# Performance work log

Hardware: AMD Instinct MI355X
Metric: run time of the kernel (lower is better)

## Reference

```python
import jax, jax.numpy as jnp
import numpy as np

N = 2708
IN_CH = 1433
OUT_CH = 128
NEG_SLOPE = 0.2


def setup_inputs() -> dict:
    key = jax.random.key(0)
    ks = jax.random.split(key, 7)
    X = jax.random.normal(ks[0], (N, IN_CH), dtype=jnp.float32)
    A = jax.random.randint(ks[1], (N, N), 0, 2, dtype=jnp.int32)
    U = jax.random.normal(ks[2], (N, N), dtype=jnp.float32)
    W = jax.random.normal(ks[3], (OUT_CH, IN_CH), dtype=jnp.float32) * (1.0 / np.sqrt(IN_CH))
    a1 = jax.random.normal(ks[4], (1, OUT_CH), dtype=jnp.float32) * (1.0 / np.sqrt(OUT_CH))
    a2 = jax.random.normal(ks[5], (1, OUT_CH), dtype=jnp.float32) * (1.0 / np.sqrt(OUT_CH))
    lmbd = jax.random.normal(ks[6], (N, 1), dtype=jnp.float32)
    return {"X": X, "A": A, "U": U, "W": W, "a1": a1, "a2": a2, "lmbd": lmbd}


def reference(X, A, U, W, a1, a2, lmbd):
    # K = W(X): [N, out]
    K = X @ W.T
    k1 = K @ a1.T                      # [N, 1]
    k2 = K @ a2.T                      # [N, 1]
    E = k1 + k2.T                      # [N, N] broadcast sum
    # spectral filter: igft(lmbd * gft(E)) = U @ (lmbd * (U^T @ E))
    E = jnp.abs(U @ (lmbd * (U.T @ E)))
    E = jnp.where(E >= 0, E, NEG_SLOPE * E)  # leaky_relu
    E_masked = jnp.where(A == 0, -jnp.inf, E)
    alpha = jax.nn.softmax(E_masked, axis=-1)  # row-wise masked softmax
    # dropout p=0.0 (eval) -> identity
    H = alpha @ K                      # [N, out]
    return H
```

## Files before the change

kernel.cpp:

```cpp
#include <hip/hip_runtime.h>
#include <math.h>

#define NN 2708
#define IC 1433
#define OC 128
#define NV (NN / 4)
#define NNOC ((size_t)NN * OC)
#define NW 85

__global__ __launch_bounds__(256) void prep2(const float* __restrict__ W, float* __restrict__ Wt,
                                             const float* __restrict__ a1, const float* __restrict__ a2,
                                             double* __restrict__ w1, double* __restrict__ w2,
                                             double* __restrict__ zd, int nzd) {
  __shared__ float tile[32][33];
  const int b = blockIdx.x, t = threadIdx.x;
  if (b < 180) {
    const int k0 = (b % 45) * 32, o0 = (b / 45) * 32;
#pragma unroll
    for (int it = 0; it < 4; it++) {
      int ro = (t >> 5) + it * 8;
      int k  = k0 + (t & 31);
      tile[ro][t & 31] = (k < IC) ? W[(size_t)(o0 + ro) * IC + k] : 0.f;
    }
    __syncthreads();
#pragma unroll
    for (int it = 0; it < 4; it++) {
      int rk = (t >> 5) + it * 8;
      int k  = k0 + rk;
      if (k < IC) Wt[(size_t)k * OC + o0 + (t & 31)] = tile[t & 31][rk];
    }
  } else if (b < 186) {
    float* a1s = &tile[0][0];
    float* a2s = a1s + 128;
    if (t < 128) { a1s[t] = a1[t]; a2s[t] = a2[t]; }
    __syncthreads();
    int c = (b - 180) * 256 + t;
    if (c < IC) {
      const float* Wc = W + c;
      double s1 = 0.0, s2 = 0.0;
#pragma unroll 4
      for (int o = 0; o < OC; o++) {
        double w = (double)Wc[(size_t)o * IC];
        s1 = fma(w, (double)a1s[o], s1);
        s2 = fma(w, (double)a2s[o], s2);
      }
      w1[c] = s1; w2[c] = s2;
    }
  } else {
    int gid = (b - 186) * 256 + t;
    if (gid < nzd) zd[gid] = 0.0;
  }
}

__global__ __launch_bounds__(256) void xw_gemm(const float* __restrict__ X,
                                               const double* __restrict__ w1, const double* __restrict__ w2,
                                               double* __restrict__ k1, double* __restrict__ k2,
                                               const float* __restrict__ Wt, float* __restrict__ Kp,
                                               const int* __restrict__ A, unsigned* __restrict__ bm,
                                               int chunk, int nsplit) {
  __shared__ __align__(16) char smem[21504];
  const int b = blockIdx.x, t = threadIdx.x;
  const int ngm = 85 * nsplit;
  if (b < ngm) {
    float (*Xs)[36]  = (float (*)[36])smem;
    float (*Ws)[132] = (float (*)[132])(smem + 32 * 36 * 4);
    const int bx = b % 85, by = b / 85;
    const int rb = bx * 32;
    const int ks = by * chunk;
    const int ke = min(IC, ks + chunk);
    float* __restrict__ Ko = Kp + (size_t)by * NNOC;
    const int row0 = (t >> 5) * 4;
    const int col4 = (t & 31) * 4;
    float acc[4][4];
#pragma unroll
    for (int r = 0; r < 4; r++)
#pragma unroll
      for (int c = 0; c < 4; c++) acc[r][c] = 0.f;

    for (int kb = ks; kb < ke; kb += 32) {
#pragma unroll
      for (int it = 0; it < 4; it++) {
        int idx = t + it * 256;
        int r = idx >> 5, c = idx & 31;
        int gr = rb + r, gc = kb + c;
        Xs[r][c] = (gr < NN && gc < ke) ? X[(size_t)gr * IC + gc] : 0.f;
      }
#pragma unroll
      for (int it = 0; it < 4; it++) {
        int idx4 = t + it * 256;
        int k = idx4 >> 5, cg = (idx4 & 31) * 4;
        int gk = kb + k;
        float4 v = make_float4(0.f, 0.f, 0.f, 0.f);
        if (gk < ke) v = *reinterpret_cast<const float4*>(&Wt[(size_t)gk * OC + cg]);
        *reinterpret_cast<float4*>(&Ws[k][cg]) = v;
      }
      __syncthreads();
#pragma unroll
      for (int g = 0; g < 8; g++) {
        float xr[4][4];
#pragma unroll
        for (int r = 0; r < 4; r++)
          *reinterpret_cast<float4*>(xr[r]) = *reinterpret_cast<const float4*>(&Xs[row0 + r][g * 4]);
#pragma unroll
        for (int j = 0; j < 4; j++) {
          const float4 w4 = *reinterpret_cast<const float4*>(&Ws[g * 4 + j][col4]);
#pragma unroll
          for (int r = 0; r < 4; r++) {
            acc[r][0] = fmaf(xr[r][j], w4.x, acc[r][0]);
            acc[r][1] = fmaf(xr[r][j], w4.y, acc[r][1]);
            acc[r][2] = fmaf(xr[r][j], w4.z, acc[r][2]);
            acc[r][3] = fmaf(xr[r][j], w4.w, acc[r][3]);
          }
        }
      }
      __syncthreads();
    }
#pragma unroll
    for (int r = 0; r < 4; r++) {
      int gr = rb + row0 + r;
      if (gr < NN) {
        float4 v = make_float4(acc[r][0], acc[r][1], acc[r][2], acc[r][3]);
        *reinterpret_cast<float4*>(&Ko[(size_t)gr * OC + col4]) = v;
      }
    }
  } else if (b < ngm + 900) {
    const int bb = b - ngm;
    int gid = bb * 256 + t;
    const int total = NN * NW;
    if (gid >= total) return;
    int i = gid / NW, w = gid - i * NW;
    const int* Ar = A + (size_t)i * NN + w * 32;
    unsigned word = 0;
    if (w < NW - 1) {
      const int4* a4 = (const int4*)Ar;
#pragma unroll
      for (int u = 0; u < 8; u++) {
        int4 a = a4[u];
        word |= (a.x != 0 ? 1u : 0u) << (4 * u);
        word |= (a.y != 0 ? 1u : 0u) << (4 * u + 1);
        word |= (a.z != 0 ? 1u : 0u) << (4 * u + 2);
        word |= (a.w != 0 ? 1u : 0u) << (4 * u + 3);
      }
    } else {
      const int nbits = NN - w * 32;
      for (int bb2 = 0; bb2 < nbits; bb2++) word |= (Ar[bb2] != 0 ? 1u : 0u) << bb2;
    }
    bm[(size_t)i * NW + w] = word;
  } else {
    const int bb = b - ngm - 900;
    const int wave = t >> 6, lane = t & 63;
    const int i = bb * 4 + wave;
    if (i >= NN) return;
    const float* Xi = X + (size_t)i * IC;
    double s1 = 0.0, s2 = 0.0;
    for (int c = lane; c < IC; c += 64) {
      double x = (double)Xi[c];
      s1 = fma(x, w1[c], s1);
      s2 = fma(x, w2[c], s2);
    }
    for (int o = 32; o; o >>= 1) { s1 += __shfl_down(s1, o, 64); s2 += __shfl_down(s2, o, 64); }
    if (lane == 0) { k1[i] = s1; k2[i] = s2; }
  }
}

__global__ __launch_bounds__(256) void mid(const float4* __restrict__ U4, const double* __restrict__ k1,
                                           double* __restrict__ u1, double* __restrict__ s,
                                           const float4* __restrict__ Kp4, float4* __restrict__ Kf4,
                                           int nsplit) {
  const int b = blockIdx.x, t = threadIdx.x;
  if (b < 255) {
    const int slab = b / 3, chunk = b - slab * 3;
    const int c4 = chunk * 256 + t;
    if (c4 >= NV) return;
    const int r0 = slab * 32;
    const int r1 = min(NN, r0 + 32);
    double au0 = 0, au1_ = 0, au2 = 0, au3 = 0, as0 = 0, as1 = 0, as2 = 0, as3 = 0;
#pragma unroll 4
    for (int r = r0; r < r1; r++) {
      float4 u = U4[(size_t)r * NV + c4];
      double kr = k1[r];
      au0 = fma((double)u.x, kr, au0); au1_ = fma((double)u.y, kr, au1_);
      au2 = fma((double)u.z, kr, au2); au3 = fma((double)u.w, kr, au3);
      as0 += (double)u.x; as1 += (double)u.y; as2 += (double)u.z; as3 += (double)u.w;
    }
    int c = c4 * 4;
    atomicAdd(&u1[c + 0], au0); atomicAdd(&u1[c + 1], au1_);
    atomicAdd(&u1[c + 2], au2); atomicAdd(&u1[c + 3], au3);
    atomicAdd(&s[c + 0], as0);  atomicAdd(&s[c + 1], as1);
    atomicAdd(&s[c + 2], as2);  atomicAdd(&s[c + 3], as3);
  } else {
    size_t i = (size_t)(b - 255) * 256 + t;
    const size_t n4 = NNOC / 4;
    if (i >= n4) return;
    float4 sv;
    if (nsplit == 4) {
      float4 v[4];
#pragma unroll
      for (int pp = 0; pp < 4; pp++) v[pp] = Kp4[(size_t)pp * n4 + i];
      sv = v[0];
#pragma unroll
      for (int pp = 1; pp < 4; pp++) {
        sv.x += v[pp].x; sv.y += v[pp].y; sv.z += v[pp].z; sv.w += v[pp].w;
      }
    } else {
      sv = Kp4[i];
      for (int pp = 1; pp < nsplit; pp++) {
        float4 v = Kp4[(size_t)pp * n4 + i];
        sv.x += v.x; sv.y += v.y; sv.z += v.z; sv.w += v.w;
      }
    }
    Kf4[i] = sv;
  }
}

__global__ __launch_bounds__(256) void softuvH(const unsigned* __restrict__ bm,
                                               const float4* __restrict__ U4, const float4* __restrict__ L4,
                                               const double2* __restrict__ u1d, const double2* __restrict__ sd,
                                               const double* __restrict__ k2,
                                               const float* __restrict__ K, float* __restrict__ H) {
  __shared__ float vf[NN];
  __shared__ short js[NN];
  __shared__ float hpart[4][128];
  __shared__ unsigned bmr[NW];
  __shared__ double redd[4], redp[4], redq[4];
  __shared__ float redf[4];
  __shared__ int cntS;

  const int i = blockIdx.x;
  const int t = threadIdx.x;
  const int wv = t >> 6, lane = t & 63;
  const unsigned long long ltmask = (1ull << lane) - 1ull;

  if (t < NW) bmr[t] = bm[(size_t)i * NW + t];
  if (t == 0) cntS = 0;

  const float4* Ur = U4 + (size_t)i * NV;
  double ap = 0.0, aq = 0.0;
  for (int c4 = t; c4 < NV; c4 += 256) {
    float4 u = Ur[c4];
    float4 lm = L4[c4];
    double2 ua = u1d[c4 * 2], ub = u1d[c4 * 2 + 1];
    double2 sa = sd[c4 * 2],  sb = sd[c4 * 2 + 1];
    ap = fma((double)u.x, (double)lm.x * ua.x, ap);
    ap = fma((double)u.y, (double)lm.y * ua.y, ap);
    ap = fma((double)u.z, (double)lm.z * ub.x, ap);
    ap = fma((double)u.w, (double)lm.w * ub.y, ap);
    aq = fma((double)u.x, (double)lm.x * sa.x, aq);
    aq = fma((double)u.y, (double)lm.y * sa.y, aq);
    aq = fma((double)u.z, (double)lm.z * sb.x, aq);
    aq = fma((double)u.w, (double)lm.w * sb.y, aq);
  }
  for (int o = 32; o; o >>= 1) { ap += __shfl_down(ap, o, 64); aq += __shfl_down(aq, o, 64); }
  if (lane == 0) { redp[wv] = ap; redq[wv] = aq; }
  __syncthreads();
  const double pi = (redp[0] + redp[1]) + (redp[2] + redp[3]);
  const double qi = (redq[0] + redq[1]) + (redq[2] + redq[3]);

  double m = -1e300;
  for (int j = t; j < NN; j += 256) {
    if ((bmr[j >> 5] >> (j & 31)) & 1u) {
      double v = fma(qi, k2[j], pi);
      m = fmax(m, fabs(v));
    }
  }
  for (int o = 32; o; o >>= 1) m = fmax(m, __shfl_xor(m, o, 64));
  if (lane == 0) redd[wv] = m;
  __syncthreads();
  m = fmax(fmax(redd[0], redd[1]), fmax(redd[2], redd[3]));

  const double thr = m - 21.0;
  float sw = 0.f;
  for (int j = t; j < NN; j += 256) {
    bool keep = false;
    double av = 0.0;
    if ((bmr[j >> 5] >> (j & 31)) & 1u) {
      av = fabs(fma(qi, k2[j], pi));
      keep = (av > thr);
    }
    unsigned long long mask = __ballot(keep);
    if (mask) {
      int src = __ffsll(mask) - 1;
      int basew = 0;
      if (lane == src) basew = atomicAdd(&cntS, __popcll(mask));
      basew = __shfl(basew, src, 64);
      if (keep) {
        int pos = basew + __popcll(mask & ltmask);
        float w = __expf((float)(av - m));
        js[pos] = (short)j;
        vf[pos] = w;
        sw += w;
      }
    }
  }
  for (int o = 32; o; o >>= 1) sw += __shfl_xor(sw, o, 64);
  if (lane == 0) redf[wv] = sw;
  __syncthreads();
  const float sumw = (redf[0] + redf[1]) + (redf[2] + redf[3]);
  const int nlist = cntS;

  const int ch = t & 63, g = t >> 6;
  float a0 = 0.f, a1 = 0.f;
  int c = g;
  for (; c + 28 < nlist; c += 32) {
    float wr[8]; int jr[8];
#pragma unroll
    for (int u = 0; u < 8; u++) { wr[u] = vf[c + 4 * u]; jr[u] = js[c + 4 * u]; }
    float kl[8], kh[8];
#pragma unroll
    for (int u = 0; u < 8; u++) {
      const float* Kr = K + (size_t)jr[u] * OC;
      kl[u] = Kr[ch]; kh[u] = Kr[64 + ch];
    }
#pragma unroll
    for (int u = 0; u < 8; u++) { a0 = fmaf(wr[u], kl[u], a0); a1 = fmaf(wr[u], kh[u], a1); }
  }
  for (; c < nlist; c += 4) {
    float w = vf[c];
    const float* Kr = K + (size_t)js[c] * OC;
    a0 = fmaf(w, Kr[ch], a0);
    a1 = fmaf(w, Kr[64 + ch], a1);
  }
  hpart[g][ch] = a0;
  hpart[g][64 + ch] = a1;
  __syncthreads();
  if (t < 128) {
    float hv = (hpart[0][t] + hpart[1][t]) + (hpart[2][t] + hpart[3][t]);
    H[(size_t)i * OC + t] = hv / sumw;
  }
}

extern "C" void kernel_launch(void* const* d_in, const int* in_sizes, int n_in,
                              void* d_out, int out_size, void* d_ws, size_t ws_size,
                              hipStream_t stream) {
  const float* X    = (const float*)d_in[0];
  const int*   A    = (const int*)d_in[1];
  const float* U    = (const float*)d_in[2];
  const float* W    = (const float*)d_in[3];
  const float* a1   = (const float*)d_in[4];
  const float* a2   = (const float*)d_in[5];
  const float* lmbd = (const float*)d_in[6];
  float* H = (float*)d_out;

  const size_t wt_bytes  = (size_t)IC * OC * 4;
  const size_t bm_bytes  = (size_t)NN * NW * 4;
  const size_t dbl_bytes = (size_t)(6 * NN + 2 * IC) * 8;

  const int splits[3] = {4, 2, 1};
  int nsplit = 1;
  for (int ci = 0; ci < 3; ci++) {
    int ns = splits[ci];
    size_t need = (size_t)(ns > 1 ? ns + 1 : 1) * NNOC * 4 + wt_bytes + dbl_bytes +
                  bm_bytes + 1024;
    if (need <= ws_size) { nsplit = ns; break; }
  }

  char* base = (char*)d_ws;
  float* Kp = (float*)base;
  float* Kf = (nsplit > 1) ? (float*)(base + (size_t)nsplit * NNOC * 4) : Kp;
  size_t off = (size_t)(nsplit > 1 ? nsplit + 1 : 1) * NNOC * 4;
  float* Wt = (float*)(base + off);            off += wt_bytes;
  double* dbl = (double*)(base + off);         off += dbl_bytes;
  double* k1  = dbl;
  double* k2  = k1 + NN;
  double* u1  = k2 + NN;
  double* sC  = u1 + NN;
  double* w1  = sC + NN + 2 * NN;
  double* w2  = w1 + IC;
  unsigned* bm = (unsigned*)(base + off);      off += bm_bytes;

  const int chunk = (IC + nsplit - 1) / nsplit;
  const int nmerge = (int)((NNOC / 4 + 255) / 256);

  prep2<<<208, 256, 0, stream>>>(W, Wt, a1, a2, w1, w2, u1, 2 * NN);
  xw_gemm<<<85 * nsplit + 900 + 677, 256, 0, stream>>>(X, w1, w2, k1, k2, Wt, Kp, A, bm,
                                                       chunk, nsplit);
  mid<<<255 + (nsplit > 1 ? nmerge : 0), 256, 0, stream>>>((const float4*)U, k1, u1, sC,
                                                           (const float4*)Kp, (float4*)Kf, nsplit);
  softuvH<<<NN, 256, 0, stream>>>(bm, (const float4*)U, (const float4*)lmbd,
                                  (const double2*)u1, (const double2*)sC, k2, Kf, H);
}
```

Baseline: 211.1 us.

## Split-K GEMM into 16 chunks with atomic accumulation, drop merge pass

Raises the split-K factor of the X·W GEMM from at most 4 to 16 (chunk of 90 along K). Partial results are now accumulated with float atomics into a buffer that prep2 zeroes, so the separate partial-sum merge in mid and its workspace go away. The k1/k2 row reduction also stages w1/w2 in shared memory. This gives more GEMM blocks for occupancy, but adds heavy float atomic traffic and makes the summation order nondeterministic.

```diff
diff --git a/kernel.cpp b/kernel.cpp
--- a/kernel.cpp
+++ b/kernel.cpp
@@ -7,11 +7,13 @@
 #define NV (NN / 4)
 #define NNOC ((size_t)NN * OC)
 #define NW 85
+#define NSPLIT 16
+#define CHUNK 90
 
 __global__ __launch_bounds__(256) void prep2(const float* __restrict__ W, float* __restrict__ Wt,
                                              const float* __restrict__ a1, const float* __restrict__ a2,
                                              double* __restrict__ w1, double* __restrict__ w2,
-                                             double* __restrict__ zd, int nzd) {
+                                             double* __restrict__ zd, float4* __restrict__ Kf4) {
   __shared__ float tile[32][33];
   const int b = blockIdx.x, t = threadIdx.x;
   if (b < 180) {
@@ -46,29 +48,30 @@
       }
       w1[c] = s1; w2[c] = s2;
     }
+  } else if (b < 208) {
+    int gid = (b - 186) * 256 + t;
+    if (gid < 2 * NN) zd[gid] = 0.0;
   } else {
-    int gid = (b - 186) * 256 + t;
-    if (gid < nzd) zd[gid] = 0.0;
+    size_t gid = (size_t)(b - 208) * 256 + t;
+    if (gid < NNOC / 4) Kf4[gid] = make_float4(0.f, 0.f, 0.f, 0.f);
   }
 }
 
 __global__ __launch_bounds__(256) void xw_gemm(const float* __restrict__ X,
                                                const double* __restrict__ w1, const double* __restrict__ w2,
                                                double* __restrict__ k1, double* __restrict__ k2,
-                                               const float* __restrict__ Wt, float* __restrict__ Kp,
-                                               const int* __restrict__ A, unsigned* __restrict__ bm,
-                                               int chunk, int nsplit) {
-  __shared__ __align__(16) char smem[21504];
+                                               const float* __restrict__ Wt, float* __restrict__ Kf,
+                                               const int* __restrict__ A, unsigned* __restrict__ bm) {
+  __shared__ __align__(16) char smem[23040];
   const int b = blockIdx.x, t = threadIdx.x;
-  const int ngm = 85 * nsplit;
+  const int ngm = 85 * NSPLIT;
   if (b < ngm) {
     float (*Xs)[36]  = (float (*)[36])smem;
     float (*Ws)[132] = (float (*)[132])(smem + 32 * 36 * 4);
     const int bx = b % 85, by = b / 85;
     const int rb = bx * 32;
-    const int ks = by * chunk;
-    const int ke = min(IC, ks + chunk);
-    float* __restrict__ Ko = Kp + (size_t)by * NNOC;
+    const int ks = by * CHUNK;
+    const int ke = min(IC, ks + CHUNK);
     const int row0 = (t >> 5) * 4;
     const int col4 = (t & 31) * 4;
     float acc[4][4];
@@ -119,8 +122,9 @@
     for (int r = 0; r < 4; r++) {
       int gr = rb + row0 + r;
       if (gr < NN) {
-        float4 v = make_float4(acc[r][0], acc[r][1], acc[r][2], acc[r][3]);
-        *reinterpret_cast<float4*>(&Ko[(size_t)gr * OC + col4]) = v;
+        float* Ko = &Kf[(size_t)gr * OC + col4];
+#pragma unroll
+        for (int cc = 0; cc < 4; cc++) atomicAdd(&Ko[cc], acc[r][cc]);
       }
     }
   } else if (b < ngm + 900) {
@@ -148,6 +152,10 @@
     bm[(size_t)i * NW + w] = word;
   } else {
     const int bb = b - ngm - 900;
+    double* w1s = (double*)smem;
+    double* w2s = w1s + IC;
+    for (int c = t; c < IC; c += 256) { w1s[c] = w1[c]; w2s[c] = w2[c]; }
+    __syncthreads();
     const int wave = t >> 6, lane = t & 63;
     const int i = bb * 4 + wave;
     if (i >= NN) return;
@@ -155,8 +163,8 @@
     double s1 = 0.0, s2 = 0.0;
     for (int c = lane; c < IC; c += 64) {
       double x = (double)Xi[c];
-      s1 = fma(x, w1[c], s1);
-      s2 = fma(x, w2[c], s2);
+      s1 = fma(x, w1s[c], s1);
+      s2 = fma(x, w2s[c], s2);
     }
     for (int o = 32; o; o >>= 1) { s1 += __shfl_down(s1, o, 64); s2 += __shfl_down(s2, o, 64); }
     if (lane == 0) { k1[i] = s1; k2[i] = s2; }
@@ -164,53 +172,27 @@
 }
 
 __global__ __launch_bounds__(256) void mid(const float4* __restrict__ U4, const double* __restrict__ k1,
-                                           double* __restrict__ u1, double* __restrict__ s,
-                                           const float4* __restrict__ Kp4, float4* __restrict__ Kf4,
-                                           int nsplit) {
+                                           double* __restrict__ u1, double* __restrict__ s) {
   const int b = blockIdx.x, t = threadIdx.x;
-  if (b < 255) {
-    const int slab = b / 3, chunk = b - slab * 3;
-    const int c4 = chunk * 256 + t;
-    if (c4 >= NV) return;
-    const int r0 = slab * 32;
-    const int r1 = min(NN, r0 + 32);
-    double au0 = 0, au1_ = 0, au2 = 0, au3 = 0, as0 = 0, as1 = 0, as2 = 0, as3 = 0;
+  const int slab = b / 3, chunk = b - slab * 3;
+  const int c4 = chunk * 256 + t;
+  if (c4 >= NV) return;
+  const int r0 = slab * 32;
+  const int r1 = min(NN, r0 + 32);
+  double au0 = 0, au1_ = 0, au2 = 0, au3 = 0, as0 = 0, as1 = 0, as2 = 0, as3 = 0;
 #pragma unroll 4
-    for (int r = r0; r < r1; r++) {
-      float4 u = U4[(size_t)r * NV + c4];
-      double kr = k1[r];
-      au0 = fma((double)u.x, kr, au0); au1_ = fma((double)u.y, kr, au1_);
-      au2 = fma((double)u.z, kr, au2); au3 = fma((double)u.w, kr, au3);
-      as0 += (double)u.x; as1 += (double)u.y; as2 += (double)u.z; as3 += (double)u.w;
-    }
-    int c = c4 * 4;
-    atomicAdd(&u1[c + 0], au0); atomicAdd(&u1[c + 1], au1_);
-    atomicAdd(&u1[c + 2], au2); atomicAdd(&u1[c + 3], au3);
-    atomicAdd(&s[c + 0], as0);  atomicAdd(&s[c + 1], as1);
-    atomicAdd(&s[c + 2], as2);  atomicAdd(&s[c + 3], as3);
-  } else {
-    size_t i = (size_t)(b - 255) * 256 + t;
-    const size_t n4 = NNOC / 4;
-    if (i >= n4) return;
-    float4 sv;
-    if (nsplit == 4) {
-      float4 v[4];
-#pragma unroll
-      for (int pp = 0; pp < 4; pp++) v[pp] = Kp4[(size_t)pp * n4 + i];
-      sv = v[0];
-#pragma unroll
-      for (int pp = 1; pp < 4; pp++) {
-        sv.x += v[pp].x; sv.y += v[pp].y; sv.z += v[pp].z; sv.w += v[pp].w;
-      }
-    } else {
-      sv = Kp4[i];
-      for (int pp = 1; pp < nsplit; pp++) {
-        float4 v = Kp4[(size_t)pp * n4 + i];
-        sv.x += v.x; sv.y += v.y; sv.z += v.z; sv.w += v.w;
-      }
-    }
-    Kf4[i] = sv;
-  }
+  for (int r = r0; r < r1; r++) {
+    float4 u = U4[(size_t)r * NV + c4];
+    double kr = k1[r];
+    au0 = fma((double)u.x, kr, au0); au1_ = fma((double)u.y, kr, au1_);
+    au2 = fma((double)u.z, kr, au2); au3 = fma((double)u.w, kr, au3);
+    as0 += (double)u.x; as1 += (double)u.y; as2 += (double)u.z; as3 += (double)u.w;
+  }
+  int c = c4 * 4;
+  atomicAdd(&u1[c + 0], au0); atomicAdd(&u1[c + 1], au1_);
+  atomicAdd(&u1[c + 2], au2); atomicAdd(&u1[c + 3], au3);
+  atomicAdd(&s[c + 0], as0);  atomicAdd(&s[c + 1], as1);
+  atomicAdd(&s[c + 2], as2);  atomicAdd(&s[c + 3], as3);
 }
 
 __global__ __launch_bounds__(256) void softuvH(const unsigned* __restrict__ bm,
@@ -341,41 +323,22 @@
   const float* lmbd = (const float*)d_in[6];
   float* H = (float*)d_out;
 
-  const size_t wt_bytes  = (size_t)IC * OC * 4;
-  const size_t bm_bytes  = (size_t)NN * NW * 4;
-  const size_t dbl_bytes = (size_t)(6 * NN + 2 * IC) * 8;
-
-  const int splits[3] = {4, 2, 1};
-  int nsplit = 1;
-  for (int ci = 0; ci < 3; ci++) {
-    int ns = splits[ci];
-    size_t need = (size_t)(ns > 1 ? ns + 1 : 1) * NNOC * 4 + wt_bytes + dbl_bytes +
-                  bm_bytes + 1024;
-    if (need <= ws_size) { nsplit = ns; break; }
-  }
-
   char* base = (char*)d_ws;
-  float* Kp = (float*)base;
-  float* Kf = (nsplit > 1) ? (float*)(base + (size_t)nsplit * NNOC * 4) : Kp;
-  size_t off = (size_t)(nsplit > 1 ? nsplit + 1 : 1) * NNOC * 4;
-  float* Wt = (float*)(base + off);            off += wt_bytes;
-  double* dbl = (double*)(base + off);         off += dbl_bytes;
+  float* Kf = (float*)base;
+  size_t off = NNOC * 4;
+  float* Wt = (float*)(base + off);            off += (size_t)IC * OC * 4;
+  double* dbl = (double*)(base + off);         off += (size_t)(6 * NN + 2 * IC) * 8;
   double* k1  = dbl;
   double* k2  = k1 + NN;
   double* u1  = k2 + NN;
   double* sC  = u1 + NN;
   double* w1  = sC + NN + 2 * NN;
   double* w2  = w1 + IC;
-  unsigned* bm = (unsigned*)(base + off);      off += bm_bytes;
-
-  const int chunk = (IC + nsplit - 1) / nsplit;
-  const int nmerge = (int)((NNOC / 4 + 255) / 256);
-
-  prep2<<<208, 256, 0, stream>>>(W, Wt, a1, a2, w1, w2, u1, 2 * NN);
-  xw_gemm<<<85 * nsplit + 900 + 677, 256, 0, stream>>>(X, w1, w2, k1, k2, Wt, Kp, A, bm,
-                                                       chunk, nsplit);
-  mid<<<255 + (nsplit > 1 ? nmerge : 0), 256, 0, stream>>>((const float4*)U, k1, u1, sC,
-                                                           (const float4*)Kp, (float4*)Kf, nsplit);
+  unsigned* bm = (unsigned*)(base + off);      off += (size_t)NN * NW * 4;
+
+  prep2<<<547, 256, 0, stream>>>(W, Wt, a1, a2, w1, w2, u1, (float4*)Kf);
+  xw_gemm<<<85 * NSPLIT + 900 + 677, 256, 0, stream>>>(X, w1, w2, k1, k2, Wt, Kf, A, bm);
+  mid<<<255, 256, 0, stream>>>((const float4*)U, k1, u1, sC);
   softuvH<<<NN, 256, 0, stream>>>(bm, (const float4*)U, (const float4*)lmbd,
                                   (const double2*)u1, (const double2*)sC, k2, Kf, H);
 }
```

After: 253.6 us. +20.1%, slower.
